# Kernel tuning notes

Measured on AMD Instinct MI355X. Metric: run time of the kernel, lower is better.

## Reference

```python
import jax, jax.numpy as jnp
import numpy as np

NP_CONST = 48.0  # Np in the original code


def dft_matrices(freq=48, time=512):
    # A[t, f] = exp(-2j*pi*t*f/time)/sqrt(time), split into re/im, shape [time, freq]
    t = np.arange(time)[:, None]
    f = np.arange(freq)[None, :]
    ang = -2.0 * np.pi * t * f / time
    scale = 1.0 / np.sqrt(time)
    return (np.cos(ang) * scale).astype(np.float32), (np.sin(ang) * scale).astype(np.float32)


def _mm(xr, xi, wr, wi):
    # complex matmul: (xr + i xi) @ (wr + i wi)
    return xr @ wr - xi @ wi, xr @ wi + xi @ wr


def _act(R, sigma, theta):
    # scaled soft-threshold (standard LAMP shrinkage); returns f and df/dR
    lam = theta[0] * sigma
    mag = jnp.abs(R)
    shr = jnp.maximum(mag - lam, 0.0)
    f = theta[1] * jnp.sign(R) * shr
    df = theta[1] * (mag > lam).astype(R.dtype)
    return f, df


def setup_inputs() -> dict:
    key = jax.random.key(0)
    L, B = 8, 8192
    dre, dim = dft_matrices(48, 512)
    u = jax.random.normal(key, (B, 48, 2), dtype=jnp.float32)
    # per-layer params initialized to the DFT matrices (as in LAMP_layer.__init__)
    A_re = jnp.broadcast_to(jnp.asarray(dre), (L, 512, 48)).copy()
    A_im = jnp.broadcast_to(jnp.asarray(dim), (L, 512, 48)).copy()
    theta = jnp.broadcast_to(jnp.array([1.0, 1.0, -1.0], dtype=jnp.float32), (L, 3)).copy()
    return {"u": u, "A_re": A_re, "A_im": A_im, "theta": theta,
            "DFT_re": jnp.asarray(dre), "DFT_im": jnp.asarray(dim)}


def _lamp_forward(u, A_re, A_im, theta, DFT_re, DFT_im):
    u_re, u_im = u[:, :, 0], u[:, :, 1]          # [B, 48]
    B = u_re.shape[0]
    z_re, z_im = u_re, u_im
    H_re = jnp.zeros((B, 512), dtype=u.dtype)
    H_im = jnp.zeros((B, 512), dtype=u.dtype)

    def layer(carry, params):
        z_re, z_im, H_re, H_im = carry
        Are, Aim, th = params                      # [512,48], [512,48], [3]
        # Z = z @ A.T : [B,48] x [48,512]
        Z_re, Z_im = _mm(z_re, z_im, Are.T, Aim.T)
        R_re = H_re + Z_re
        R_im = H_im + Z_im
        sigma = jnp.sqrt(jnp.sum(z_re * z_re) + jnp.sum(z_im * z_im)) / jnp.sqrt(NP_CONST)
        Hn_re, d_re = _act(R_re, sigma, th)
        Hn_im, d_im = _act(R_im, sigma, th)
        b_re = d_re.sum() / NP_CONST
        b_im = d_im.sum() / NP_CONST
        # h_hat = H_hat @ A : [B,512] x [512,48]
        h_re, h_im = _mm(Hn_re, Hn_im, Are, Aim)
        zn_re = u_re - h_re + b_re * z_re
        zn_im = u_im - h_im + b_im * z_im
        return (zn_re, zn_im, Hn_re, Hn_im), None

    (z_re, z_im, H_re, H_im), _ = jax.lax.scan(layer, (z_re, z_im, H_re, H_im),
                                               (A_re, A_im, theta))
    h_re, h_im = _mm(H_re, H_im, DFT_re, DFT_im)   # [B, 48]
    return jnp.stack((h_re, h_im), axis=2)          # [B, 48, 2]


def reference(u, A_re, A_im, theta, DFT_re, DFT_im):
    return _lamp_forward(u, A_re, A_im, theta, DFT_re, DFT_im)
```

## Files before the change

### kernel.cpp

```cpp
#include <hip/hip_runtime.h>
#include <hip/hip_bf16.h>
#include <math.h>

#define B_   8192
#define F_   48
#define T_   512
#define L_   8
#define NBLK 256
#define THR  512
#define NW   8
#define RPB  32
#define HST  520
#define ZS   52
#define LINE 32
#define NEVT 15
#define NGRP 16
#define GSZ  16
#define MAXV 6
#define VALS_OFF ((NGRP + 1) * LINE)
#define SYNC_DW  (VALS_OFF + NEVT * MAXV * NBLK)

typedef unsigned short ushort_t;
typedef unsigned int   uint_t;
typedef __attribute__((ext_vector_type(8))) short short8;
typedef __attribute__((ext_vector_type(4))) float f32x4;

#define MFMA(a,b,c) __builtin_amdgcn_mfma_f32_16x16x32_bf16(a,b,c,0,0,0)

__device__ inline ushort_t f2bf(float x) {
    __hip_bfloat16 h = __float2bfloat16(x);
    return *reinterpret_cast<ushort_t*>(&h);
}
__device__ inline short8 negbf(short8 v) {
    short8 r;
    #pragma unroll
    for (int i = 0; i < 8; ++i) r[i] = v[i] ^ (short)0x8000;
    return r;
}
__device__ inline short8 pack8(float4 a, float4 b) {
    short8 r;
    r[0]=(short)f2bf(a.x); r[1]=(short)f2bf(a.y); r[2]=(short)f2bf(a.z); r[3]=(short)f2bf(a.w);
    r[4]=(short)f2bf(b.x); r[5]=(short)f2bf(b.y); r[6]=(short)f2bf(b.z); r[7]=(short)f2bf(b.w);
    return r;
}

__device__ inline float aload(const float* p) {
    return __hip_atomic_load(p, __ATOMIC_RELAXED, __HIP_MEMORY_SCOPE_AGENT);
}
__device__ inline void astore(float* p, float v) {
    __hip_atomic_store(p, v, __ATOMIC_RELAXED, __HIP_MEMORY_SCOPE_AGENT);
}

__global__ __launch_bounds__(256) void k_pre(
    const float* __restrict__ Ar, const float* __restrict__ Ai,
    const float* __restrict__ Dr, const float* __restrict__ Di,
    ushort_t* __restrict__ Afr, ushort_t* __restrict__ Afi,
    ushort_t* __restrict__ Atr, ushort_t* __restrict__ Ati,
    ushort_t* __restrict__ Dfr, ushort_t* __restrict__ Dfi,
    uint_t* __restrict__ syncbuf)
{
    const int gt = blockIdx.x * 256 + threadIdx.x;
    const int gs = gridDim.x * 256;
    if (gt < VALS_OFF) syncbuf[gt] = 0u;
    for (int idx = gt; idx < L_ * 32768; idx += gs) {
        int j = idx & 7, rest = idx >> 3;
        int mm = rest & 15; rest >>= 4;
        int qq = rest & 3;  rest >>= 2;
        int k2 = rest & 1;  rest >>= 1;
        int tile = rest & 31;
        int l = rest >> 5;
        int t = tile * 16 + mm, k = k2 * 32 + qq * 8 + j;
        float vr = 0.f, vi = 0.f;
        if (k < 48) { int g = l * 24576 + t * 48 + k; vr = Ar[g]; vi = Ai[g]; }
        Afr[idx] = f2bf(vr); Afi[idx] = f2bf(vi);
    }
    for (int idx = gt; idx < L_ * 24576; idx += gs) {
        int j = idx & 7, rest = idx >> 3;
        int mm = rest & 15; rest >>= 4;
        int qq = rest & 3;  rest >>= 2;
        int ks = rest & 15; rest >>= 4;
        int ft = rest % 3;
        int l = rest / 3;
        int f = ft * 16 + mm, k = ks * 32 + qq * 8 + j;
        int g = l * 24576 + k * 48 + f;
        Atr[idx] = f2bf(Ar[g]); Ati[idx] = f2bf(Ai[g]);
    }
    for (int idx = gt; idx < 24576; idx += gs) {
        int j = idx & 7, rest = idx >> 3;
        int mm = rest & 15; rest >>= 4;
        int qq = rest & 3;  rest >>= 2;
        int ks = rest & 15;
        int ft = rest >> 4;
        int f = ft * 16 + mm, k = ks * 32 + qq * 8 + j;
        Dfr[idx] = f2bf(Dr[k * 48 + f]); Dfi[idx] = f2bf(Di[k * 48 + f]);
    }
}

__global__ __launch_bounds__(THR, 2) void k_lamp(
    const float* __restrict__ u,
    const ushort_t* __restrict__ Afr, const ushort_t* __restrict__ Afi,
    const ushort_t* __restrict__ Atr, const ushort_t* __restrict__ Ati,
    const ushort_t* __restrict__ Dfr, const ushort_t* __restrict__ Dfi,
    const float* __restrict__ th,
    uint_t* syncbuf,
    float* __restrict__ out)
{
    extern __shared__ char dyn[];
    float*    pR   = (float*)dyn;
    float*    pI   = pR + 8 * 3 * 16 * 17;
    float*    zreL = pI + 8 * 3 * 16 * 17;
    float*    zimL = zreL + RPB * ZS;
    float*    red  = zimL + RPB * ZS;
    ushort_t* HreL = (ushort_t*)(red + 128);
    ushort_t* HimL = HreL + RPB * HST;

    uint_t* leaf = syncbuf;
    uint_t* root = syncbuf + NGRP * LINE;
    float*  vals = (float*)syncbuf + VALS_OFF;

    const int tid = threadIdx.x, blk = blockIdx.x;
    const int grp = blk >> 4;
    const int row0 = blk * RPB;
    const int wave = tid >> 6, lane = tid & 63;
    const int quad = lane >> 4, m = lane & 15;
    const int rows16 = (wave >> 2) * 16;
    const int rt = wave >> 2, kq = wave & 3;
    const float2* u2 = (const float2*)u;

    auto publishv = [&](int e, const float* v, int nv) {
        float* base = vals + (size_t)e * MAXV * NBLK;
        for (int j = 0; j < nv; ++j) astore(base + j * NBLK + blk, v[j]);
        uint_t old = __hip_atomic_fetch_add(&leaf[grp * LINE], 1u,
                                            __ATOMIC_ACQ_REL, __HIP_MEMORY_SCOPE_AGENT);
        if (old == (uint_t)(GSZ * (e + 1)) - 1u)
            (void)__hip_atomic_fetch_add(root, 1u, __ATOMIC_RELEASE,
                                         __HIP_MEMORY_SCOPE_AGENT);
    };
    auto consume = [&](int e, int nv) {
        if (tid == 0) {
            uint_t tgt = (uint_t)NGRP * (uint_t)(e + 1);
            int spin = 0;
            while (__hip_atomic_load(root, __ATOMIC_RELAXED,
                                     __HIP_MEMORY_SCOPE_AGENT) < tgt) {
                if (++spin > 8) __builtin_amdgcn_s_sleep(1);
            }
            (void)__hip_atomic_load(root, __ATOMIC_ACQUIRE,
                                    __HIP_MEMORY_SCOPE_AGENT);
        }
        __syncthreads();
        if (wave < nv) {
            const float* base = vals + (size_t)e * MAXV * NBLK + (size_t)wave * NBLK;
            float s = 0.f;
            #pragma unroll
            for (int g = 0; g < NBLK / 64; ++g) s += aload(base + g * 64 + lane);
            #pragma unroll
            for (int o = 32; o > 0; o >>= 1) s += __shfl_xor(s, o, 64);
            if (lane == 0) red[wave] = s;
        }
        __syncthreads();
    };

    f32x4 hR[8], hI[8];
    #pragma unroll
    for (int ct = 0; ct < 8; ++ct) { hR[ct] = (f32x4){0,0,0,0}; hI[ct] = (f32x4){0,0,0,0}; }

    float uRe[3], uIm[3];
    float acc = 0.f;
    #pragma unroll
    for (int k3 = 0; k3 < 3; ++k3) {
        int j = tid + k3 * THR;
        int r = j / 48, c = j - r * 48;
        float2 v = u2[(row0 + r) * 48 + c];
        uRe[k3] = v.x; uIm[k3] = v.y;
        zreL[r * ZS + c] = v.x; zimL[r * ZS + c] = v.y;
        acc += v.x * v.x + v.y * v.y;
    }
    #pragma unroll
    for (int o = 32; o > 0; o >>= 1) acc += __shfl_xor(acc, o, 64);
    __syncthreads();
    if (lane == 0) red[16 + wave] = acc;
    __syncthreads();
    if (tid == 0) {
        float t = 0.f;
        #pragma unroll
        for (int w = 0; w < NW; ++w) t += red[16 + w];
        publishv(0, &t, 1);
    }

    float lam = 0.f, bre = 0.f, bim = 0.f;
    for (int l = 0; l < L_; ++l) {
        const float th1 = th[l * 3 + 1];

        const float* zpr = zreL + (rows16 + m) * ZS;
        const float* zpi = zimL + (rows16 + m) * ZS;
        short8 zr0 = pack8(*(const float4*)(zpr + quad * 8), *(const float4*)(zpr + quad * 8 + 4));
        short8 zi0 = pack8(*(const float4*)(zpi + quad * 8), *(const float4*)(zpi + quad * 8 + 4));
        short8 zr1 = {0,0,0,0,0,0,0,0}, zi1 = {0,0,0,0,0,0,0,0};
        if (quad < 2) {
            zr1 = pack8(*(const float4*)(zpr + 32 + quad * 8), *(const float4*)(zpr + 36 + quad * 8));
            zi1 = pack8(*(const float4*)(zpi + 32 + quad * 8), *(const float4*)(zpi + 36 + quad * 8));
        }
        short8 zin0 = negbf(zi0), zin1 = negbf(zi1);

        const ushort_t* Aflr = Afr + (size_t)l * 32768;
        const ushort_t* Afli = Afi + (size_t)l * 32768;
        #pragma unroll
        for (int ct = 0; ct < 8; ++ct) {
            const int tile = (wave & 3) * 8 + ct;
            const ushort_t* rp = Aflr + (size_t)(tile * 2) * 512 + lane * 8;
            const ushort_t* ip = Afli + (size_t)(tile * 2) * 512 + lane * 8;
            short8 ar0 = *(const short8*)rp;
            short8 ar1 = *(const short8*)(rp + 512);
            short8 ai0 = *(const short8*)ip;
            short8 ai1 = *(const short8*)(ip + 512);
            hR[ct] = MFMA(zr0, ar0, hR[ct]);
            hR[ct] = MFMA(zr1, ar1, hR[ct]);
            hR[ct] = MFMA(zin0, ai0, hR[ct]);
            hR[ct] = MFMA(zin1, ai1, hR[ct]);
            hI[ct] = MFMA(zr0, ai0, hI[ct]);
            hI[ct] = MFMA(zr1, ai1, hI[ct]);
            hI[ct] = MFMA(zi0, ar0, hI[ct]);
            hI[ct] = MFMA(zi1, ar1, hI[ct]);
        }

        if (l == 0) {
            consume(0, 1);
            lam = th[0] * sqrtf(red[0] * (1.0f / 48.0f));
        } else {
            consume(2 * l, 6);
            float sig2 = red[0] + 2.f * bre * red[1] + bre * bre * red[2]
                       + red[3] + 2.f * bim * red[4] + bim * bim * red[5];
            lam = th[l * 3] * sqrtf(sig2 * (1.0f / 48.0f));
        }

        float cr = 0.f, ci = 0.f;
        #pragma unroll
        for (int ct = 0; ct < 8; ++ct) {
            const int t = ((wave & 3) * 8 + ct) * 16 + m;
            #pragma unroll
            for (int reg = 0; reg < 4; ++reg) {
                const int lr = rows16 + quad * 4 + reg;
                float Rr = hR[ct][reg], Ri = hI[ct][reg];
                float mr = fabsf(Rr), mi = fabsf(Ri);
                float fr = th1 * copysignf(fmaxf(mr - lam, 0.f), Rr);
                float fi = th1 * copysignf(fmaxf(mi - lam, 0.f), Ri);
                cr += (mr > lam) ? 1.f : 0.f;
                ci += (mi > lam) ? 1.f : 0.f;
                hR[ct][reg] = fr; hI[ct][reg] = fi;
                HreL[lr * HST + t] = f2bf(fr);
                HimL[lr * HST + t] = f2bf(fi);
            }
        }

        if (l == L_ - 1) { __syncthreads(); break; }

        #pragma unroll
        for (int o = 32; o > 0; o >>= 1) { cr += __shfl_xor(cr, o, 64); ci += __shfl_xor(ci, o, 64); }
        if (lane == 0) { red[16 + wave] = cr; red[24 + wave] = ci; }
        __syncthreads();
        if (tid == 0) {
            float v2[2] = {0.f, 0.f};
            #pragma unroll
            for (int w = 0; w < NW; ++w) { v2[0] += red[16 + w]; v2[1] += red[24 + w]; }
            publishv(2 * l + 1, v2, 2);
        }

        const ushort_t* Atlr = Atr + (size_t)l * 24576;
        const ushort_t* Atli = Ati + (size_t)l * 24576;
        f32x4 aR[3], aI[3];
        #pragma unroll
        for (int q = 0; q < 3; ++q) { aR[q] = (f32x4){0,0,0,0}; aI[q] = (f32x4){0,0,0,0}; }
        #pragma unroll
        for (int ks = 0; ks < 4; ++ks) {
            const int ksa = kq * 4 + ks;
            const int k0 = ksa * 32 + quad * 8;
            short8 hr = *(const short8*)&HreL[(rt * 16 + m) * HST + k0];
            short8 hi = *(const short8*)&HimL[(rt * 16 + m) * HST + k0];
            short8 hin = negbf(hi);
            #pragma unroll
            for (int ft = 0; ft < 3; ++ft) {
                short8 br = *(const short8*)(Atlr + (size_t)((ft * 16 + ksa) * 64 + lane) * 8);
                short8 bi = *(const short8*)(Atli + (size_t)((ft * 16 + ksa) * 64 + lane) * 8);
                aR[ft] = MFMA(hr, br, aR[ft]);
                aR[ft] = MFMA(hin, bi, aR[ft]);
                aI[ft] = MFMA(hr, bi, aI[ft]);
                aI[ft] = MFMA(hi, br, aI[ft]);
            }
        }
        #pragma unroll
        for (int ft = 0; ft < 3; ++ft) {
            #pragma unroll
            for (int reg = 0; reg < 4; ++reg) {
                pR[((wave * 3 + ft) * 16 + quad * 4 + reg) * 17 + m] = aR[ft][reg];
                pI[((wave * 3 + ft) * 16 + quad * 4 + reg) * 17 + m] = aI[ft][reg];
            }
        }
        __syncthreads();

        consume(2 * l + 1, 2);
        bre = th1 * red[0] * (1.0f / 48.0f);
        bim = th1 * red[1] * (1.0f / 48.0f);

        float aRe[3], aIm[3], zR3[3], zI3[3];
        float S1 = 0.f, S2 = 0.f, S3 = 0.f, S4 = 0.f, S5 = 0.f, S6 = 0.f;
        #pragma unroll
        for (int k3 = 0; k3 < 3; ++k3) {
            int j = tid + k3 * THR;
            int r = j / 48, f = j - r * 48;
            int rt2 = r >> 4, lr = r & 15, ft = f >> 4, c = f & 15;
            float hRv = 0.f, hIv = 0.f;
            #pragma unroll
            for (int q = 0; q < 4; ++q) {
                hRv += pR[(((rt2 * 4 + q) * 3 + ft) * 16 + lr) * 17 + c];
                hIv += pI[(((rt2 * 4 + q) * 3 + ft) * 16 + lr) * 17 + c];
            }
            float zr = zreL[r * ZS + f], zi = zimL[r * ZS + f];
            float ar = uRe[k3] - hRv, ai = uIm[k3] - hIv;
            aRe[k3] = ar; aIm[k3] = ai; zR3[k3] = zr; zI3[k3] = zi;
            S1 += ar * ar; S2 += ar * zr; S3 += zr * zr;
            S4 += ai * ai; S5 += ai * zi; S6 += zi * zi;
        }

        float v6[6] = {S1, S2, S3, S4, S5, S6};
        #pragma unroll
        for (int j = 0; j < 6; ++j) {
            #pragma unroll
            for (int o = 32; o > 0; o >>= 1) v6[j] += __shfl_xor(v6[j], o, 64);
        }
        if (lane == 0) {
            #pragma unroll
            for (int j = 0; j < 6; ++j) red[16 + wave * 6 + j] = v6[j];
        }
        __syncthreads();
        if (tid == 0) {
            float o6[6];
            #pragma unroll
            for (int j = 0; j < 6; ++j) {
                float s = 0.f;
                #pragma unroll
                for (int w = 0; w < NW; ++w) s += red[16 + w * 6 + j];
                o6[j] = s;
            }
            publishv(2 * l + 2, o6, 6);
        }

        #pragma unroll
        for (int k3 = 0; k3 < 3; ++k3) {
            int j = tid + k3 * THR;
            int r = j / 48, f = j - r * 48;
            zreL[r * ZS + f] = aRe[k3] + bre * zR3[k3];
            zimL[r * ZS + f] = aIm[k3] + bim * zI3[k3];
        }
        __syncthreads();
    }

    f32x4 fR[3], fI[3];
    #pragma unroll
    for (int q = 0; q < 3; ++q) { fR[q] = (f32x4){0,0,0,0}; fI[q] = (f32x4){0,0,0,0}; }
    #pragma unroll
    for (int ks = 0; ks < 4; ++ks) {
        const int ksa = kq * 4 + ks;
        const int k0 = ksa * 32 + quad * 8;
        short8 hr = *(const short8*)&HreL[(rt * 16 + m) * HST + k0];
        short8 hi = *(const short8*)&HimL[(rt * 16 + m) * HST + k0];
        short8 hin = negbf(hi);
        #pragma unroll
        for (int ft = 0; ft < 3; ++ft) {
            short8 br = *(const short8*)(Dfr + (size_t)((ft * 16 + ksa) * 64 + lane) * 8);
            short8 bi = *(const short8*)(Dfi + (size_t)((ft * 16 + ksa) * 64 + lane) * 8);
            fR[ft] = MFMA(hr, br, fR[ft]);
            fR[ft] = MFMA(hin, bi, fR[ft]);
            fI[ft] = MFMA(hr, bi, fI[ft]);
            fI[ft] = MFMA(hi, br, fI[ft]);
        }
    }
    #pragma unroll
    for (int ft = 0; ft < 3; ++ft) {
        #pragma unroll
        for (int reg = 0; reg < 4; ++reg) {
            pR[((wave * 3 + ft) * 16 + quad * 4 + reg) * 17 + m] = fR[ft][reg];
            pI[((wave * 3 + ft) * 16 + quad * 4 + reg) * 17 + m] = fI[ft][reg];
        }
    }
    __syncthreads();
    float2* out2 = (float2*)out;
    #pragma unroll
    for (int k3 = 0; k3 < 3; ++k3) {
        int j = tid + k3 * THR;
        int r = j / 48, f = j - r * 48;
        int rt2 = r >> 4, lr = r & 15, ft = f >> 4, c = f & 15;
        float hRv = 0.f, hIv = 0.f;
        #pragma unroll
        for (int q = 0; q < 4; ++q) {
            hRv += pR[(((rt2 * 4 + q) * 3 + ft) * 16 + lr) * 17 + c];
            hIv += pI[(((rt2 * 4 + q) * 3 + ft) * 16 + lr) * 17 + c];
        }
        out2[(row0 + r) * 48 + f] = make_float2(hRv, hIv);
    }
}

extern "C" void kernel_launch(void* const* d_in, const int* in_sizes, int n_in,
                              void* d_out, int out_size, void* d_ws, size_t ws_size,
                              hipStream_t stream) {
    (void)in_sizes; (void)n_in; (void)out_size; (void)ws_size;
    const float* u  = (const float*)d_in[0];
    const float* Ar = (const float*)d_in[1];
    const float* Ai = (const float*)d_in[2];
    const float* th = (const float*)d_in[3];
    const float* Dr = (const float*)d_in[4];
    const float* Di = (const float*)d_in[5];
    float* out = (float*)d_out;

    char* p = (char*)d_ws;
    auto alloc = [&](size_t bytes) -> char* {
        char* r = p;
        p += (bytes + 255) & ~(size_t)255;
        return r;
    };
    uint_t*   syncbuf = (uint_t*)alloc((size_t)SYNC_DW * 4);
    ushort_t* Afr = (ushort_t*)alloc((size_t)L_ * 32768 * 2);
    ushort_t* Afi = (ushort_t*)alloc((size_t)L_ * 32768 * 2);
    ushort_t* Atr = (ushort_t*)alloc((size_t)L_ * 24576 * 2);
    ushort_t* Ati = (ushort_t*)alloc((size_t)L_ * 24576 * 2);
    ushort_t* Dfr = (ushort_t*)alloc((size_t)24576 * 2);
    ushort_t* Dfi = (ushort_t*)alloc((size_t)24576 * 2);

    k_pre<<<512, 256, 0, stream>>>(Ar, Ai, Dr, Di, Afr, Afi, Atr, Ati, Dfr, Dfi, syncbuf);

    const uint_t lds_bytes = 132608;
    hipFuncSetAttribute((const void*)k_lamp,
                        hipFuncAttributeMaxDynamicSharedMemorySize, (int)lds_bytes);
    k_lamp<<<dim3(NBLK), dim3(THR), lds_bytes, stream>>>(
        u, Afr, Afi, Atr, Ati, Dfr, Dfi, th, syncbuf, out);
}
```

Baseline: 298.0 us.

## Split grid barrier into two counter chains and defer b-coefficient consume

Uses two separate leaf/root counter trees for the two kinds of grid-wide reduction events, so the b-coefficient event and the sigma-statistics event are counted independently. The consume of the b values now happens after the sigma-statistics partials are computed and published, so the grid-wide wait overlaps with the reduction work instead of blocking before it. The spin loop also always sleeps. This relies on the sigma statistics being expressible without b, which the code already does by publishing six moments. It risks ordering or visibility bugs if the separate counters are not synchronised correctly.

```diff
diff --git a/kernel.cpp b/kernel.cpp
--- a/kernel.cpp
+++ b/kernel.cpp
@@ -17,8 +17,11 @@
 #define NGRP 16
 #define GSZ  16
 #define MAXV 6
-#define VALS_OFF ((NGRP + 1) * LINE)
-#define SYNC_DW  (VALS_OFF + NEVT * MAXV * NBLK)
+#define ROOTA_OFF (NGRP * LINE)
+#define LEAFB_OFF ((NGRP + 1) * LINE)
+#define ROOTB_OFF ((2 * NGRP + 1) * LINE)
+#define VALS_OFF  ((2 * NGRP + 2) * LINE)
+#define SYNC_DW   (VALS_OFF + NEVT * MAXV * NBLK)
 
 typedef unsigned short ushort_t;
 typedef unsigned int   uint_t;
@@ -114,9 +117,11 @@
     ushort_t* HreL = (ushort_t*)(red + 128);
     ushort_t* HimL = HreL + RPB * HST;
 
-    uint_t* leaf = syncbuf;
-    uint_t* root = syncbuf + NGRP * LINE;
-    float*  vals = (float*)syncbuf + VALS_OFF;
+    uint_t* leafA = syncbuf;
+    uint_t* rootA = syncbuf + ROOTA_OFF;
+    uint_t* leafB = syncbuf + LEAFB_OFF;
+    uint_t* rootB = syncbuf + ROOTB_OFF;
+    float*  vals  = (float*)syncbuf + VALS_OFF;
 
     const int tid = threadIdx.x, blk = blockIdx.x;
     const int grp = blk >> 4;
@@ -127,29 +132,34 @@
     const int rt = wave >> 2, kq = wave & 3;
     const float2* u2 = (const float2*)u;
 
-    auto publishv = [&](int e, const float* v, int nv) {
-        float* base = vals + (size_t)e * MAXV * NBLK;
-        for (int j = 0; j < nv; ++j) astore(base + j * NBLK + blk, v[j]);
-        uint_t old = __hip_atomic_fetch_add(&leaf[grp * LINE], 1u,
-                                            __ATOMIC_ACQ_REL, __HIP_MEMORY_SCOPE_AGENT);
-        if (old == (uint_t)(GSZ * (e + 1)) - 1u)
+    auto arrive = [&](uint_t* leaf, uint_t* root, int k) {
+        uint_t* lf = leaf + (size_t)grp * LINE;
+        uint_t old = __hip_atomic_fetch_add(lf, 1u, __ATOMIC_RELEASE,
+                                            __HIP_MEMORY_SCOPE_AGENT);
+        if (old == (uint_t)(GSZ * (k + 1)) - 1u) {
+            (void)__hip_atomic_load(lf, __ATOMIC_ACQUIRE, __HIP_MEMORY_SCOPE_AGENT);
             (void)__hip_atomic_fetch_add(root, 1u, __ATOMIC_RELEASE,
                                          __HIP_MEMORY_SCOPE_AGENT);
+        }
     };
-    auto consume = [&](int e, int nv) {
+    auto publishv = [&](uint_t* leaf, uint_t* root, int k, int evidx,
+                        const float* v, int nv) {
+        float* base = vals + (size_t)evidx * MAXV * NBLK;
+        for (int j = 0; j < nv; ++j) astore(base + j * NBLK + blk, v[j]);
+        arrive(leaf, root, k);
+    };
+    auto consume = [&](uint_t* root, int k, int evidx, int nv) {
         if (tid == 0) {
-            uint_t tgt = (uint_t)NGRP * (uint_t)(e + 1);
-            int spin = 0;
+            uint_t tgt = (uint_t)NGRP * (uint_t)(k + 1);
             while (__hip_atomic_load(root, __ATOMIC_RELAXED,
-                                     __HIP_MEMORY_SCOPE_AGENT) < tgt) {
-                if (++spin > 8) __builtin_amdgcn_s_sleep(1);
-            }
+                                     __HIP_MEMORY_SCOPE_AGENT) < tgt)
+                __builtin_amdgcn_s_sleep(2);
             (void)__hip_atomic_load(root, __ATOMIC_ACQUIRE,
                                     __HIP_MEMORY_SCOPE_AGENT);
         }
         __syncthreads();
         if (wave < nv) {
-            const float* base = vals + (size_t)e * MAXV * NBLK + (size_t)wave * NBLK;
+            const float* base = vals + (size_t)evidx * MAXV * NBLK + (size_t)wave * NBLK;
             float s = 0.f;
             #pragma unroll
             for (int g = 0; g < NBLK / 64; ++g) s += aload(base + g * 64 + lane);
@@ -184,7 +194,7 @@
         float t = 0.f;
         #pragma unroll
         for (int w = 0; w < NW; ++w) t += red[16 + w];
-        publishv(0, &t, 1);
+        publishv(leafB, rootB, 0, 0, &t, 1);
     }
 
     float lam = 0.f, bre = 0.f, bim = 0.f;
@@ -224,10 +234,10 @@
         }
 
         if (l == 0) {
-            consume(0, 1);
+            consume(rootB, 0, 0, 1);
             lam = th[0] * sqrtf(red[0] * (1.0f / 48.0f));
         } else {
-            consume(2 * l, 6);
+            consume(rootB, l, 2 * l, 6);
             float sig2 = red[0] + 2.f * bre * red[1] + bre * bre * red[2]
                        + red[3] + 2.f * bim * red[4] + bim * bim * red[5];
             lam = th[l * 3] * sqrtf(sig2 * (1.0f / 48.0f));
@@ -262,7 +272,7 @@
             float v2[2] = {0.f, 0.f};
             #pragma unroll
             for (int w = 0; w < NW; ++w) { v2[0] += red[16 + w]; v2[1] += red[24 + w]; }
-            publishv(2 * l + 1, v2, 2);
+            publishv(leafA, rootA, l, 2 * l + 1, v2, 2);
         }
 
         const ushort_t* Atlr = Atr + (size_t)l * 24576;
@@ -296,10 +306,6 @@
             }
         }
         __syncthreads();
-
-        consume(2 * l + 1, 2);
-        bre = th1 * red[0] * (1.0f / 48.0f);
-        bim = th1 * red[1] * (1.0f / 48.0f);
 
         float aRe[3], aIm[3], zR3[3], zI3[3];
         float S1 = 0.f, S2 = 0.f, S3 = 0.f, S4 = 0.f, S5 = 0.f, S6 = 0.f;
@@ -341,8 +347,12 @@
                 for (int w = 0; w < NW; ++w) s += red[16 + w * 6 + j];
                 o6[j] = s;
             }
-            publishv(2 * l + 2, o6, 6);
-        }
+            publishv(leafB, rootB, l + 1, 2 * l + 2, o6, 6);
+        }
+
+        consume(rootA, l, 2 * l + 1, 2);
+        bre = th1 * red[0] * (1.0f / 48.0f);
+        bim = th1 * red[1] * (1.0f / 48.0f);
 
         #pragma unroll
         for (int k3 = 0; k3 < 3; ++k3) {
```

After: 303.5 us. No clear change (+1.8%).
